# Kernel tuning notes

Measured on AMD Instinct MI355X. Metric: run time of the kernel, lower is better.

The kernel has to match this reference:

```python
import jax, jax.numpy as jnp
import numpy as np


def setup_inputs() -> dict:
    key = jax.random.key(0)
    k_x, k_m, k_w1, k_b1, k_w2, k_b2 = jax.random.split(key, 6)
    b, seq_len, d_in, d_out = 8, 4096, 1024, 512
    x = jax.random.normal(k_x, (b, seq_len, d_in), dtype=jnp.float32)
    # binary-ish mask in {0,1} as floats (torch code multiplies by mask)
    mask = (jax.random.uniform(k_m, (b, seq_len)) < 0.5).astype(jnp.float32)
    s1 = 1.0 / np.sqrt(d_in)
    s2 = 1.0 / np.sqrt(d_out)
    W_enc = jax.random.uniform(k_w1, (d_out, d_in), minval=-s1, maxval=s1, dtype=jnp.float32)
    b_enc = jax.random.uniform(k_b1, (d_out,), minval=-s1, maxval=s1, dtype=jnp.float32)
    W_dec = jax.random.uniform(k_w2, (d_in, d_out), minval=-s2, maxval=s2, dtype=jnp.float32)
    b_dec = jax.random.uniform(k_b2, (d_in,), minval=-s2, maxval=s2, dtype=jnp.float32)
    return {"x": x, "mask": mask, "W_enc": W_enc, "b_enc": b_enc, "W_dec": W_dec, "b_dec": b_dec}


def reference(x, mask, W_enc, b_enc, W_dec, b_dec):
    # per-step: v_t = v_{t-1} + relu(x_t @ W_enc^T + b_enc) * mask_t  -> additive scan == cumsum
    h = jax.nn.relu(jnp.einsum('bsd,od->bso', x, W_enc) + b_enc) * mask[:, :, None]  # [b,s,d_out]
    v_cum = jnp.cumsum(h, axis=1)  # [b,s,d_out]
    out_enc = jnp.einsum('bso,do->bsd', v_cum, W_dec) + b_dec  # decode every prefix state
    v = v_cum[:, -1, :]  # final accumulated state
    return (v, out_enc)
```

## Files before the change

### kernel.cpp

```cpp
#include <hip/hip_runtime.h>
#include <hip/hip_bf16.h>
#include <stdint.h>

typedef __bf16 bf16_t;
typedef __bf16 bf16x4 __attribute__((ext_vector_type(4)));
typedef __bf16 bf16x8 __attribute__((ext_vector_type(8)));
typedef float  f32x4  __attribute__((ext_vector_type(4)));

__device__ __forceinline__ void gload_lds16(const void* g, void* l) {
  __builtin_amdgcn_global_load_lds(
      (__attribute__((address_space(1))) void*)g,
      (__attribute__((address_space(3))) void*)l, 16, 0, 0);
}

__global__ void cast_kernel(const float* __restrict__ in, bf16_t* __restrict__ out, int n4) {
  const int stride = gridDim.x * blockDim.x;
  for (int i = blockIdx.x * blockDim.x + threadIdx.x; i < n4; i += stride) {
    f32x4 v = reinterpret_cast<const f32x4*>(in)[i];
    bf16x4 o;
    o[0] = (bf16_t)v[0]; o[1] = (bf16_t)v[1]; o[2] = (bf16_t)v[2]; o[3] = (bf16_t)v[3];
    reinterpret_cast<bf16x4*>(out)[i] = o;
  }
}

__global__ void cast_weights(const float* __restrict__ a, bf16_t* __restrict__ oa,
                             const float* __restrict__ b, bf16_t* __restrict__ ob,
                             int n4each) {
  const int i = blockIdx.x * blockDim.x + threadIdx.x;
  const float* src; bf16_t* dst; int k;
  if (i < n4each) { src = a; dst = oa; k = i; }
  else            { src = b; dst = ob; k = i - n4each; }
  f32x4 v = reinterpret_cast<const f32x4*>(src)[k];
  bf16x4 o;
  o[0] = (bf16_t)v[0]; o[1] = (bf16_t)v[1]; o[2] = (bf16_t)v[2]; o[3] = (bf16_t)v[3];
  reinterpret_cast<bf16x4*>(dst)[k] = o;
}


#define PHASE_SYNC() do { \
  __builtin_amdgcn_s_barrier(); \
  asm volatile("s_waitcnt lgkmcnt(0)" ::: "memory"); \
  __builtin_amdgcn_sched_barrier(0); \
  __builtin_amdgcn_s_setprio(1); \
} while (0)

#define PHASE_END() do { \
  __builtin_amdgcn_s_setprio(0); \
  __builtin_amdgcn_s_barrier(); \
} while (0)

#define QUAD(RH, CH, BF) do { \
  _Pragma("unroll") \
  for (int fr = 0; fr < 4; ++fr) { \
    _Pragma("unroll") \
    for (int fc = 0; fc < 2; ++fc) { \
      acc[RH][CH][fr][fc] = __builtin_amdgcn_mfma_f32_16x16x32_bf16(a[fr][0], BF[fc][0], acc[RH][CH][fr][fc], 0, 0, 0); \
      acc[RH][CH][fr][fc] = __builtin_amdgcn_mfma_f32_16x16x32_bf16(a[fr][1], BF[fc][1], acc[RH][CH][fr][fc], 0, 0, 0); \
    } \
  } \
} while (0)

template<int EPI>
__global__ __launch_bounds__(512, 2) void gemm8p(
    const bf16_t* __restrict__ A, const bf16_t* __restrict__ B,
    const int K, const int N,
    const float* __restrict__ bias, const float* __restrict__ mask,
    const float* __restrict__ Padd,
    bf16_t* __restrict__ h_out, float* __restrict__ partials,
    float* __restrict__ outf)
{
  __shared__ __align__(16) char smem[131072];

  const int tid  = threadIdx.x;
  const int lane = tid & 63;
  const int w    = tid >> 6;
  const int wm   = w >> 2;
  const int wn   = w & 3;
  const long bm  = (long)blockIdx.x * 256;
  const long bn  = (long)blockIdx.y * 256;
  const int NT   = K >> 6;

  const int scol = (((lane & 7) ^ (lane >> 3)) << 3);
  const int fcb0 = ((((lane >> 4)    ) ^ (lane & 7)) << 3);
  const int fcb1 = ((((lane >> 4) + 4) ^ (lane & 7)) << 3);

  f32x4  acc[2][2][4][2] = {};
  bf16x8 a[4][2], b0[2][2], b1[2][2];

  auto Albs = [&](int buf) { return (bf16_t*)(smem + buf * 65536); };
  auto Blbs = [&](int buf) { return (bf16_t*)(smem + buf * 65536 + 32768); };

  auto stageA = [&](int t, int h) {
    bf16_t* lb = Albs(t & 1);
    #pragma unroll
    for (int c = 0; c < 2; ++c) {
      const int r0 = h * 128 + (w * 2 + c) * 8;
      gload_lds16(A + (bm + r0 + (lane >> 3)) * (long)K + t * 64 + scol, lb + r0 * 64);
    }
  };
  auto stageB = [&](int t, int h) {
    bf16_t* lb = Blbs(t & 1);
    #pragma unroll
    for (int c = 0; c < 2; ++c) {
      const int r0 = h * 128 + (w * 2 + c) * 8;
      gload_lds16(B + (bn + r0 + (lane >> 3)) * (long)K + t * 64 + scol, lb + r0 * 64);
    }
  };
  auto loadA = [&](int buf, int rh) {
    const bf16_t* lb = Albs(buf);
    #pragma unroll
    for (int fr = 0; fr < 4; ++fr) {
      const int row = rh * 128 + wm * 64 + fr * 16 + (lane & 15);
      a[fr][0] = *reinterpret_cast<const bf16x8*>(lb + row * 64 + fcb0);
      a[fr][1] = *reinterpret_cast<const bf16x8*>(lb + row * 64 + fcb1);
    }
  };
  auto loadB = [&](int buf, int ch, bf16x8 (&bf)[2][2]) {
    const bf16_t* lb = Blbs(buf);
    #pragma unroll
    for (int fc = 0; fc < 2; ++fc) {
      const int row = ch * 128 + wn * 32 + fc * 16 + (lane & 15);
      bf[fc][0] = *reinterpret_cast<const bf16x8*>(lb + row * 64 + fcb0);
      bf[fc][1] = *reinterpret_cast<const bf16x8*>(lb + row * 64 + fcb1);
    }
  };

  __builtin_amdgcn_sched_barrier(0);
  stageA(0, 0); stageA(0, 1); stageB(0, 0); stageB(0, 1);
  stageA(1, 0); stageB(1, 0); stageA(1, 1);
  asm volatile("s_waitcnt vmcnt(6)" ::: "memory");
  __builtin_amdgcn_s_barrier();

  for (int t = 0; t < NT; ++t) {
    const int buf = t & 1;
    const bool s2 = (t + 2 < NT);
    const bool s1 = (t + 1 < NT);

    loadA(buf, 0);
    loadB(buf, 0, b0);
    if (s1) stageB(t + 1, 1);
    PHASE_SYNC(); QUAD(0, 0, b0); PHASE_END();

    loadB(buf, 1, b1);
    if (s2) stageA(t + 2, 0);
    PHASE_SYNC(); QUAD(0, 1, b1); PHASE_END();

    loadA(buf, 1);
    if (s2) stageB(t + 2, 0);
    PHASE_SYNC(); QUAD(1, 0, b0); PHASE_END();

    if (s2) stageA(t + 2, 1);
    PHASE_SYNC(); QUAD(1, 1, b1);
    __builtin_amdgcn_s_setprio(0);
    if (s2)      { asm volatile("s_waitcnt vmcnt(6)" ::: "memory"); }
    else if (s1) { asm volatile("s_waitcnt vmcnt(0)" ::: "memory"); }
    __builtin_amdgcn_s_barrier();
  }
  __builtin_amdgcn_sched_barrier(0);

  if (EPI == 0) {
    bf16_t* tile = (bf16_t*)smem;
    float bv[2][2];
    #pragma unroll
    for (int ch = 0; ch < 2; ++ch)
      #pragma unroll
      for (int fc = 0; fc < 2; ++fc)
        bv[ch][fc] = bias[bn + ch * 128 + wn * 32 + fc * 16 + (lane & 15)];

    #pragma unroll
    for (int rh = 0; rh < 2; ++rh)
      #pragma unroll
      for (int fr = 0; fr < 4; ++fr) {
        const int row0 = rh * 128 + wm * 64 + fr * 16 + ((lane >> 4) << 2);
        const f32x4 mv = *reinterpret_cast<const f32x4*>(&mask[bm + row0]);
        #pragma unroll
        for (int ch = 0; ch < 2; ++ch)
          #pragma unroll
          for (int fc = 0; fc < 2; ++fc) {
            const int col = ch * 128 + wn * 32 + fc * 16 + (lane & 15);
            #pragma unroll
            for (int e = 0; e < 4; ++e) {
              const int row = row0 + e;
              float hv = acc[rh][ch][fr][fc][e] + bv[ch][fc];
              hv = (hv > 0.f ? hv : 0.f) * mv[e];
              tile[row * 256 + (col ^ (((row >> 2) & 3) << 4))] = (bf16_t)hv;
            }
          }
      }
    __syncthreads();

    const int sub = tid >> 8;
    const int col = tid & 255;
    float run = 0.f;
    bf16_t* hp = h_out + (bm + sub * 128) * 512 + bn + col;
    #pragma unroll 4
    for (int s = 0; s < 128; ++s) {
      const int row = sub * 128 + s;
      run += (float)tile[row * 256 + (col ^ (((row >> 2) & 3) << 4))];
      hp[(long)s * 512] = (bf16_t)run;
    }
    partials[(blockIdx.x * 2 + sub) * 512 + bn + col] = run;
  } else {
    #pragma unroll
    for (int rh = 0; rh < 2; ++rh)
      #pragma unroll
      for (int ch = 0; ch < 2; ++ch)
        #pragma unroll
        for (int fc = 0; fc < 2; ++fc) {
          const long gc = bn + ch * 128 + wn * 32 + fc * 16 + (lane & 15);
          const float pv = Padd[(blockIdx.x * 2 + rh) * (long)N + gc];
          #pragma unroll
          for (int fr = 0; fr < 4; ++fr) {
            const long gr = bm + rh * 128 + wm * 64 + fr * 16 + ((lane >> 4) << 2);
            #pragma unroll
            for (int e = 0; e < 4; ++e)
              outf[(gr + e) * (long)N + gc] = acc[rh][ch][fr][fc][e] + pv;
          }
        }
  }
}

__global__ __launch_bounds__(256) void gemm_p(
    const bf16_t* __restrict__ A, const bf16_t* __restrict__ B,
    const int K, const int N,
    const float* __restrict__ bias,
    float* __restrict__ outf)
{
  __shared__ __align__(16) bf16_t As[2][128 * 64];
  __shared__ __align__(16) bf16_t Bs[2][128 * 64];

  const int tid  = threadIdx.x;
  const int lane = tid & 63;
  const int w    = tid >> 6;
  const int wm   = w >> 1, wn = w & 1;
  const long bm  = (long)blockIdx.x * 128;
  const long bn  = (long)blockIdx.y * 128;

  f32x4 acc[4][4] = {};

  const int srow = w * 32 + (lane >> 3);
  const int scol = (lane & 7) * 8;
  const bf16_t* Abase = A + (bm + srow) * (long)K + scol;
  const bf16_t* Bbase = B + (bn + srow) * (long)K + scol;

  auto stage = [&](bf16_t* da, bf16_t* db, int kt) {
    #pragma unroll
    for (int it = 0; it < 4; ++it) {
      gload_lds16(Abase + (long)it * 8 * K + kt, &da[(w * 32 + it * 8) * 64]);
      gload_lds16(Bbase + (long)it * 8 * K + kt, &db[(w * 32 + it * 8) * 64]);
    }
  };
  auto mfma_tile = [&](const bf16_t* Asb, const bf16_t* Bsb) {
    #pragma unroll
    for (int kk = 0; kk < 2; ++kk) {
      const int kof = kk * 32 + (lane >> 4) * 8;
      bf16x8 afr[4], bfr[4];
      #pragma unroll
      for (int i = 0; i < 4; ++i)
        afr[i] = *reinterpret_cast<const bf16x8*>(&Asb[(wm * 64 + i * 16 + (lane & 15)) * 64 + kof]);
      #pragma unroll
      for (int j = 0; j < 4; ++j)
        bfr[j] = *reinterpret_cast<const bf16x8*>(&Bsb[(wn * 64 + j * 16 + (lane & 15)) * 64 + kof]);
      #pragma unroll
      for (int i = 0; i < 4; ++i)
        #pragma unroll
        for (int j = 0; j < 4; ++j)
          acc[i][j] = __builtin_amdgcn_mfma_f32_16x16x32_bf16(afr[i], bfr[j], acc[i][j], 0, 0, 0);
    }
  };

  stage(As[0], Bs[0], 0);
  __syncthreads();
  int kt = 64;
  for (int p2 = 0; p2 < (K >> 7); ++p2) {
    if (kt < K) stage(As[1], Bs[1], kt);
    mfma_tile(As[0], Bs[0]);
    __syncthreads();
    kt += 64;
    if (kt < K) stage(As[0], Bs[0], kt);
    mfma_tile(As[1], Bs[1]);
    __syncthreads();
    kt += 64;
  }

  #pragma unroll
  for (int j = 0; j < 4; ++j) {
    const long gc = bn + wn * 64 + j * 16 + (lane & 15);
    const float addv = bias[gc];
    #pragma unroll
    for (int i = 0; i < 4; ++i) {
      const long gr0 = bm + wm * 64 + i * 16 + ((lane >> 4) << 2);
      #pragma unroll
      for (int r = 0; r < 4; ++r)
        outf[(gr0 + r) * (long)N + gc] = acc[i][j][r] + addv;
    }
  }
}

__global__ void scan_chunks(const float* __restrict__ partials, bf16_t* __restrict__ prefixb,
                            float* __restrict__ v_out) {
  const int idx = blockIdx.x * blockDim.x + threadIdx.x;
  const int b = idx >> 9;
  const int o = idx & 511;
  float run = 0.f;
  #pragma unroll
  for (int c = 0; c < 32; ++c) {
    const size_t off = ((size_t)(b * 32 + c)) * 512 + o;
    prefixb[off] = (bf16_t)run;
    run += partials[off];
  }
  v_out[idx] = run;
}

extern "C" void kernel_launch(void* const* d_in, const int* in_sizes, int n_in,
                              void* d_out, int out_size, void* d_ws, size_t ws_size,
                              hipStream_t stream) {
  const float* x     = (const float*)d_in[0];
  const float* mask  = (const float*)d_in[1];
  const float* W_enc = (const float*)d_in[2];
  const float* b_enc = (const float*)d_in[3];
  const float* W_dec = (const float*)d_in[4];
  const float* b_dec = (const float*)d_in[5];

  float* out     = (float*)d_out;
  float* v_out   = out;
  float* out_enc = out + 4096;

  char* ws = (char*)d_ws;
  bf16_t* xb       = (bf16_t*)ws;  ws += (size_t)32768 * 1024 * 2;
  bf16_t* Web      = (bf16_t*)ws;  ws += (size_t)512 * 1024 * 2;
  bf16_t* Wdb      = (bf16_t*)ws;  ws += (size_t)1024 * 512 * 2;
  bf16_t* h        = (bf16_t*)ws;  ws += (size_t)32768 * 512 * 2;
  float*  partials = (float*)ws;   ws += (size_t)256 * 512 * 4;
  bf16_t* prefixb  = (bf16_t*)ws;  ws += (size_t)256 * 512 * 2;
  float*  P        = (float*)ws;   ws += (size_t)256 * 1024 * 4;

  cast_kernel<<<2048, 256, 0, stream>>>(x, xb, 33554432 / 4);
  cast_weights<<<1024, 256, 0, stream>>>(W_enc, Web, W_dec, Wdb, 131072);

  gemm8p<0><<<dim3(128, 2), 512, 0, stream>>>(xb, Web, 1024, 512,
                                              b_enc, mask, nullptr, h, partials, nullptr);

  scan_chunks<<<16, 256, 0, stream>>>(partials, prefixb, v_out);

  gemm_p<<<dim3(2, 8), 256, 0, stream>>>(prefixb, Wdb, 512, 1024, b_dec, P);

  gemm8p<1><<<dim3(128, 4), 512, 0, stream>>>(h, Wdb, 512, 1024,
                                              nullptr, nullptr, P, nullptr, nullptr, out_enc);
}
```

Baseline: 163.7 us.

## Fuse fp32-to-bf16 cast of x into the encoder GEMM's LDS staging

Drops the separate cast kernel for x. The encoder GEMM now loads fp32 x tiles directly into LDS and converts them to bf16 while reading fragments. This removes a full write and re-read of a 64 MB bf16 copy of x. In exchange, the encoder kernel moves twice the bytes per A tile through LDS, single-buffers A with a restructured staging and waitcnt schedule, and does extra conversion work in the inner loop. The decoder GEMM also has its prefetch order and wait counts reshuffled.

```diff
diff --git a/kernel.cpp b/kernel.cpp
--- a/kernel.cpp
+++ b/kernel.cpp
@@ -11,16 +11,6 @@
   __builtin_amdgcn_global_load_lds(
       (__attribute__((address_space(1))) void*)g,
       (__attribute__((address_space(3))) void*)l, 16, 0, 0);
-}
-
-__global__ void cast_kernel(const float* __restrict__ in, bf16_t* __restrict__ out, int n4) {
-  const int stride = gridDim.x * blockDim.x;
-  for (int i = blockIdx.x * blockDim.x + threadIdx.x; i < n4; i += stride) {
-    f32x4 v = reinterpret_cast<const f32x4*>(in)[i];
-    bf16x4 o;
-    o[0] = (bf16_t)v[0]; o[1] = (bf16_t)v[1]; o[2] = (bf16_t)v[2]; o[3] = (bf16_t)v[3];
-    reinterpret_cast<bf16x4*>(out)[i] = o;
-  }
 }
 
 __global__ void cast_weights(const float* __restrict__ a, bf16_t* __restrict__ oa,
@@ -36,7 +26,6 @@
   reinterpret_cast<bf16x4*>(dst)[k] = o;
 }
 
-
 #define PHASE_SYNC() do { \
   __builtin_amdgcn_s_barrier(); \
   asm volatile("s_waitcnt lgkmcnt(0)" ::: "memory"); \
@@ -60,13 +49,161 @@
   } \
 } while (0)
 
-template<int EPI>
-__global__ __launch_bounds__(512, 2) void gemm8p(
+__global__ __launch_bounds__(512, 2) void gemm1_f8p(
+    const float* __restrict__ x, const bf16_t* __restrict__ Wenc,
+    const float* __restrict__ b_enc, const float* __restrict__ mask,
+    bf16_t* __restrict__ h_out, float* __restrict__ partials)
+{
+  __shared__ __align__(16) char smem[131072];
+  float* Af = (float*)smem;
+  auto Bl = [&](int buf) { return (bf16_t*)(smem + 65536 + buf * 32768); };
+
+  const int tid  = threadIdx.x;
+  const int lane = tid & 63;
+  const int w    = tid >> 6;
+  const int wm   = w >> 2;
+  const int wn   = w & 3;
+  const long bm  = (long)blockIdx.x * 256;
+  const long bn  = (long)blockIdx.y * 256;
+  const int NT   = 16;
+
+  f32x4  acc[2][2][4][2] = {};
+  bf16x8 a[4][2], b0[2][2], b1[2][2];
+
+  const int scolB = (((lane & 7) ^ (lane >> 3)) << 3);
+  auto stageB = [&](int t, int h) {
+    bf16_t* lb = Bl(t & 1);
+    #pragma unroll
+    for (int c = 0; c < 2; ++c) {
+      const int r0 = h * 128 + (w * 2 + c) * 8;
+      gload_lds16(Wenc + (bn + r0 + (lane >> 3)) * 1024 + t * 64 + scolB, lb + r0 * 64);
+    }
+  };
+  auto stageA = [&](int t, int h) {
+    #pragma unroll
+    for (int c = 0; c < 4; ++c) {
+      const int r0  = h * 128 + w * 16 + c * 4;
+      const int row = r0 + (lane >> 4);
+      const int sblk = (lane & 15) ^ (row & 15);
+      gload_lds16(x + (bm + row) * 1024 + t * 64 + sblk * 4, Af + r0 * 64);
+    }
+  };
+  auto loadAf = [&](int rh) {
+    #pragma unroll
+    for (int fr = 0; fr < 4; ++fr) {
+      const int row = rh * 128 + wm * 64 + fr * 16 + (lane & 15);
+      const float* rp = Af + row * 64;
+      #pragma unroll
+      for (int kx = 0; kx < 2; ++kx) {
+        const int g0 = kx * 8 + (lane >> 4) * 2;
+        f32x4 lo = *reinterpret_cast<const f32x4*>(rp + (((g0    ) ^ (lane & 15)) << 2));
+        f32x4 hi = *reinterpret_cast<const f32x4*>(rp + (((g0 + 1) ^ (lane & 15)) << 2));
+        bf16x8 o;
+        #pragma unroll
+        for (int e = 0; e < 4; ++e) { o[e] = (bf16_t)lo[e]; o[e + 4] = (bf16_t)hi[e]; }
+        a[fr][kx] = o;
+      }
+    }
+  };
+  const int fcb0 = ((((lane >> 4)    ) ^ (lane & 7)) << 3);
+  const int fcb1 = ((((lane >> 4) + 4) ^ (lane & 7)) << 3);
+  auto loadB = [&](int buf, int ch, bf16x8 (&bf)[2][2]) {
+    const bf16_t* lb = Bl(buf);
+    #pragma unroll
+    for (int fc = 0; fc < 2; ++fc) {
+      const int row = ch * 128 + wn * 32 + fc * 16 + (lane & 15);
+      bf[fc][0] = *reinterpret_cast<const bf16x8*>(lb + row * 64 + fcb0);
+      bf[fc][1] = *reinterpret_cast<const bf16x8*>(lb + row * 64 + fcb1);
+    }
+  };
+
+  __builtin_amdgcn_sched_barrier(0);
+  stageA(0, 0); stageA(0, 1); stageB(0, 0); stageB(0, 1);
+  stageB(1, 0); stageB(1, 1);
+  asm volatile("s_waitcnt vmcnt(4)" ::: "memory");
+  __builtin_amdgcn_s_barrier();
+
+  for (int t = 0; t < NT; ++t) {
+    const int buf = t & 1;
+    const bool g1 = (t + 1 < NT);
+    const bool g2 = (t + 2 < NT);
+
+    loadAf(0); loadB(buf, 0, b0);
+    PHASE_SYNC(); QUAD(0, 0, b0); PHASE_END();
+
+    loadB(buf, 1, b1);
+    if (g1) stageA(t + 1, 0);
+    if (g2) stageB(t + 2, 0);
+    PHASE_SYNC(); QUAD(0, 1, b1);
+    __builtin_amdgcn_s_setprio(0);
+    if (g2)      asm volatile("s_waitcnt vmcnt(6)" ::: "memory");
+    else if (g1) asm volatile("s_waitcnt vmcnt(4)" ::: "memory");
+    else         asm volatile("s_waitcnt vmcnt(0)" ::: "memory");
+    __builtin_amdgcn_s_barrier();
+
+    loadAf(1);
+    if (g2) stageB(t + 2, 1);
+    PHASE_SYNC(); QUAD(1, 0, b0); PHASE_END();
+
+    if (g1) stageA(t + 1, 1);
+    PHASE_SYNC(); QUAD(1, 1, b1);
+    __builtin_amdgcn_s_setprio(0);
+    if (g2)      asm volatile("s_waitcnt vmcnt(8)" ::: "memory");
+    else if (g1) asm volatile("s_waitcnt vmcnt(4)" ::: "memory");
+    else         asm volatile("s_waitcnt vmcnt(0)" ::: "memory");
+    __builtin_amdgcn_s_barrier();
+  }
+  asm volatile("s_waitcnt vmcnt(0) lgkmcnt(0)" ::: "memory");
+  __builtin_amdgcn_s_barrier();
+  __builtin_amdgcn_sched_barrier(0);
+
+  bf16_t* tile = (bf16_t*)smem;
+  float bv[2][2];
+  #pragma unroll
+  for (int ch = 0; ch < 2; ++ch)
+    #pragma unroll
+    for (int fc = 0; fc < 2; ++fc)
+      bv[ch][fc] = b_enc[bn + ch * 128 + wn * 32 + fc * 16 + (lane & 15)];
+
+  #pragma unroll
+  for (int rh = 0; rh < 2; ++rh)
+    #pragma unroll
+    for (int fr = 0; fr < 4; ++fr) {
+      const int row0 = rh * 128 + wm * 64 + fr * 16 + ((lane >> 4) << 2);
+      const f32x4 mv = *reinterpret_cast<const f32x4*>(&mask[bm + row0]);
+      #pragma unroll
+      for (int ch = 0; ch < 2; ++ch)
+        #pragma unroll
+        for (int fc = 0; fc < 2; ++fc) {
+          const int col = ch * 128 + wn * 32 + fc * 16 + (lane & 15);
+          #pragma unroll
+          for (int e = 0; e < 4; ++e) {
+            const int row = row0 + e;
+            float hv = acc[rh][ch][fr][fc][e] + bv[ch][fc];
+            hv = (hv > 0.f ? hv : 0.f) * mv[e];
+            tile[row * 256 + (col ^ (((row >> 2) & 3) << 4))] = (bf16_t)hv;
+          }
+        }
+    }
+  __syncthreads();
+
+  const int sub = tid >> 8;
+  const int col = tid & 255;
+  float run = 0.f;
+  bf16_t* hp = h_out + (bm + sub * 128) * 512 + bn + col;
+  #pragma unroll 4
+  for (int s = 0; s < 128; ++s) {
+    const int row = sub * 128 + s;
+    run += (float)tile[row * 256 + (col ^ (((row >> 2) & 3) << 4))];
+    hp[(long)s * 512] = (bf16_t)run;
+  }
+  partials[(blockIdx.x * 2 + sub) * 512 + bn + col] = run;
+}
+
+__global__ __launch_bounds__(512, 2) void gemm2_8p(
     const bf16_t* __restrict__ A, const bf16_t* __restrict__ B,
     const int K, const int N,
-    const float* __restrict__ bias, const float* __restrict__ mask,
     const float* __restrict__ Padd,
-    bf16_t* __restrict__ h_out, float* __restrict__ partials,
     float* __restrict__ outf)
 {
   __shared__ __align__(16) char smem[131072];
@@ -127,97 +264,50 @@
 
   __builtin_amdgcn_sched_barrier(0);
   stageA(0, 0); stageA(0, 1); stageB(0, 0); stageB(0, 1);
-  stageA(1, 0); stageB(1, 0); stageA(1, 1);
-  asm volatile("s_waitcnt vmcnt(6)" ::: "memory");
+  stageA(1, 0); stageA(1, 1); stageB(1, 0); stageB(1, 1);
+  asm volatile("s_waitcnt vmcnt(8)" ::: "memory");
   __builtin_amdgcn_s_barrier();
 
   for (int t = 0; t < NT; ++t) {
     const int buf = t & 1;
-    const bool s2 = (t + 2 < NT);
-    const bool s1 = (t + 1 < NT);
-
-    loadA(buf, 0);
-    loadB(buf, 0, b0);
-    if (s1) stageB(t + 1, 1);
+    const bool g2 = (t + 2 < NT);
+
+    loadA(buf, 0); loadB(buf, 0, b0);
     PHASE_SYNC(); QUAD(0, 0, b0); PHASE_END();
 
     loadB(buf, 1, b1);
-    if (s2) stageA(t + 2, 0);
+    if (g2) stageA(t + 2, 0);
     PHASE_SYNC(); QUAD(0, 1, b1); PHASE_END();
 
     loadA(buf, 1);
-    if (s2) stageB(t + 2, 0);
+    if (g2) stageB(t + 2, 0);
     PHASE_SYNC(); QUAD(1, 0, b0); PHASE_END();
 
-    if (s2) stageA(t + 2, 1);
+    if (g2) { stageA(t + 2, 1); stageB(t + 2, 1); }
     PHASE_SYNC(); QUAD(1, 1, b1);
     __builtin_amdgcn_s_setprio(0);
-    if (s2)      { asm volatile("s_waitcnt vmcnt(6)" ::: "memory"); }
-    else if (s1) { asm volatile("s_waitcnt vmcnt(0)" ::: "memory"); }
+    if (g2) asm volatile("s_waitcnt vmcnt(8)" ::: "memory");
+    else    asm volatile("s_waitcnt vmcnt(0)" ::: "memory");
     __builtin_amdgcn_s_barrier();
   }
   __builtin_amdgcn_sched_barrier(0);
 
-  if (EPI == 0) {
-    bf16_t* tile = (bf16_t*)smem;
-    float bv[2][2];
+  #pragma unroll
+  for (int rh = 0; rh < 2; ++rh)
     #pragma unroll
     for (int ch = 0; ch < 2; ++ch)
       #pragma unroll
-      for (int fc = 0; fc < 2; ++fc)
-        bv[ch][fc] = bias[bn + ch * 128 + wn * 32 + fc * 16 + (lane & 15)];
-
-    #pragma unroll
-    for (int rh = 0; rh < 2; ++rh)
-      #pragma unroll
-      for (int fr = 0; fr < 4; ++fr) {
-        const int row0 = rh * 128 + wm * 64 + fr * 16 + ((lane >> 4) << 2);
-        const f32x4 mv = *reinterpret_cast<const f32x4*>(&mask[bm + row0]);
+      for (int fc = 0; fc < 2; ++fc) {
+        const long gc = bn + ch * 128 + wn * 32 + fc * 16 + (lane & 15);
+        const float pv = Padd[(blockIdx.x * 2 + rh) * (long)N + gc];
         #pragma unroll
-        for (int ch = 0; ch < 2; ++ch)
+        for (int fr = 0; fr < 4; ++fr) {
+          const long gr = bm + rh * 128 + wm * 64 + fr * 16 + ((lane >> 4) << 2);
           #pragma unroll
-          for (int fc = 0; fc < 2; ++fc) {
-            const int col = ch * 128 + wn * 32 + fc * 16 + (lane & 15);
-            #pragma unroll
-            for (int e = 0; e < 4; ++e) {
-              const int row = row0 + e;
-              float hv = acc[rh][ch][fr][fc][e] + bv[ch][fc];
-              hv = (hv > 0.f ? hv : 0.f) * mv[e];
-              tile[row * 256 + (col ^ (((row >> 2) & 3) << 4))] = (bf16_t)hv;
-            }
-          }
+          for (int e = 0; e < 4; ++e)
+            outf[(gr + e) * (long)N + gc] = acc[rh][ch][fr][fc][e] + pv;
+        }
       }
-    __syncthreads();
-
-    const int sub = tid >> 8;
-    const int col = tid & 255;
-    float run = 0.f;
-    bf16_t* hp = h_out + (bm + sub * 128) * 512 + bn + col;
-    #pragma unroll 4
-    for (int s = 0; s < 128; ++s) {
-      const int row = sub * 128 + s;
-      run += (float)tile[row * 256 + (col ^ (((row >> 2) & 3) << 4))];
-      hp[(long)s * 512] = (bf16_t)run;
-    }
-    partials[(blockIdx.x * 2 + sub) * 512 + bn + col] = run;
-  } else {
-    #pragma unroll
-    for (int rh = 0; rh < 2; ++rh)
-      #pragma unroll
-      for (int ch = 0; ch < 2; ++ch)
-        #pragma unroll
-        for (int fc = 0; fc < 2; ++fc) {
-          const long gc = bn + ch * 128 + wn * 32 + fc * 16 + (lane & 15);
-          const float pv = Padd[(blockIdx.x * 2 + rh) * (long)N + gc];
-          #pragma unroll
-          for (int fr = 0; fr < 4; ++fr) {
-            const long gr = bm + rh * 128 + wm * 64 + fr * 16 + ((lane >> 4) << 2);
-            #pragma unroll
-            for (int e = 0; e < 4; ++e)
-              outf[(gr + e) * (long)N + gc] = acc[rh][ch][fr][fc][e] + pv;
-          }
-        }
-  }
 }
 
 __global__ __launch_bounds__(256) void gemm_p(
@@ -327,7 +417,6 @@
   float* out_enc = out + 4096;
 
   char* ws = (char*)d_ws;
-  bf16_t* xb       = (bf16_t*)ws;  ws += (size_t)32768 * 1024 * 2;
   bf16_t* Web      = (bf16_t*)ws;  ws += (size_t)512 * 1024 * 2;
   bf16_t* Wdb      = (bf16_t*)ws;  ws += (size_t)1024 * 512 * 2;
   bf16_t* h        = (bf16_t*)ws;  ws += (size_t)32768 * 512 * 2;
@@ -335,16 +424,13 @@
   bf16_t* prefixb  = (bf16_t*)ws;  ws += (size_t)256 * 512 * 2;
   float*  P        = (float*)ws;   ws += (size_t)256 * 1024 * 4;
 
-  cast_kernel<<<2048, 256, 0, stream>>>(x, xb, 33554432 / 4);
   cast_weights<<<1024, 256, 0, stream>>>(W_enc, Web, W_dec, Wdb, 131072);
 
-  gemm8p<0><<<dim3(128, 2), 512, 0, stream>>>(xb, Web, 1024, 512,
-                                              b_enc, mask, nullptr, h, partials, nullptr);
+  gemm1_f8p<<<dim3(128, 2), 512, 0, stream>>>(x, Web, b_enc, mask, h, partials);
 
   scan_chunks<<<16, 256, 0, stream>>>(partials, prefixb, v_out);
 
   gemm_p<<<dim3(2, 8), 256, 0, stream>>>(prefixb, Wdb, 512, 1024, b_dec, P);
 
-  gemm8p<1><<<dim3(128, 4), 512, 0, stream>>>(h, Wdb, 512, 1024,
-                                              nullptr, nullptr, P, nullptr, nullptr, out_enc);
-}
+  gemm2_8p<<<dim3(128, 4), 512, 0, stream>>>(h, Wdb, 512, 1024, P, out_enc);
+}
```

New measurement: 138.9 us. -15.2%, faster.

## Merge cast kernels and restage GEMM prefetch to two tiles ahead

Applied to the files above, without the earlier changes.

The x and weight casts are folded into one grid-stride kernel, which removes a launch. The GEMM prefetch schedule changes so that both halves of A and B for tile t+2 are staged within iteration t, replacing the mixed t+1/t+2 staging. The vmcnt thresholds are adjusted to match, and an lgkmcnt wait is added before the first quad. This aims to simplify and deepen the load pipeline, but more loads stay in flight, and wrong wait counts could stall the loop or break correctness.

```diff
diff --git a/kernel.cpp b/kernel.cpp
--- a/kernel.cpp
+++ b/kernel.cpp
@@ -13,29 +13,23 @@
       (__attribute__((address_space(3))) void*)l, 16, 0, 0);
 }
 
-__global__ void cast_kernel(const float* __restrict__ in, bf16_t* __restrict__ out, int n4) {
+__global__ void cast_all(const float* __restrict__ x, bf16_t* __restrict__ xb,
+                         const float* __restrict__ we, bf16_t* __restrict__ web,
+                         const float* __restrict__ wd, bf16_t* __restrict__ wdb) {
+  const int NX = 8388608;
+  const int NW = 131072;
   const int stride = gridDim.x * blockDim.x;
-  for (int i = blockIdx.x * blockDim.x + threadIdx.x; i < n4; i += stride) {
-    f32x4 v = reinterpret_cast<const f32x4*>(in)[i];
+  for (int i = blockIdx.x * blockDim.x + threadIdx.x; i < NX + 2 * NW; i += stride) {
+    const float* src; bf16_t* dst; int k;
+    if (i < NX)           { src = x;  dst = xb;  k = i; }
+    else if (i < NX + NW) { src = we; dst = web; k = i - NX; }
+    else                  { src = wd; dst = wdb; k = i - NX - NW; }
+    f32x4 v = reinterpret_cast<const f32x4*>(src)[k];
     bf16x4 o;
     o[0] = (bf16_t)v[0]; o[1] = (bf16_t)v[1]; o[2] = (bf16_t)v[2]; o[3] = (bf16_t)v[3];
-    reinterpret_cast<bf16x4*>(out)[i] = o;
-  }
-}
-
-__global__ void cast_weights(const float* __restrict__ a, bf16_t* __restrict__ oa,
-                             const float* __restrict__ b, bf16_t* __restrict__ ob,
-                             int n4each) {
-  const int i = blockIdx.x * blockDim.x + threadIdx.x;
-  const float* src; bf16_t* dst; int k;
-  if (i < n4each) { src = a; dst = oa; k = i; }
-  else            { src = b; dst = ob; k = i - n4each; }
-  f32x4 v = reinterpret_cast<const f32x4*>(src)[k];
-  bf16x4 o;
-  o[0] = (bf16_t)v[0]; o[1] = (bf16_t)v[1]; o[2] = (bf16_t)v[2]; o[3] = (bf16_t)v[3];
-  reinterpret_cast<bf16x4*>(dst)[k] = o;
-}
-
+    reinterpret_cast<bf16x4*>(dst)[k] = o;
+  }
+}
 
 #define PHASE_SYNC() do { \
   __builtin_amdgcn_s_barrier(); \
@@ -127,33 +121,31 @@
 
   __builtin_amdgcn_sched_barrier(0);
   stageA(0, 0); stageA(0, 1); stageB(0, 0); stageB(0, 1);
-  stageA(1, 0); stageB(1, 0); stageA(1, 1);
-  asm volatile("s_waitcnt vmcnt(6)" ::: "memory");
+  stageA(1, 0); stageA(1, 1); stageB(1, 0); stageB(1, 1);
+  asm volatile("s_waitcnt vmcnt(8)" ::: "memory");
   __builtin_amdgcn_s_barrier();
 
   for (int t = 0; t < NT; ++t) {
     const int buf = t & 1;
-    const bool s2 = (t + 2 < NT);
-    const bool s1 = (t + 1 < NT);
-
-    loadA(buf, 0);
-    loadB(buf, 0, b0);
-    if (s1) stageB(t + 1, 1);
+    const bool g2 = (t + 2 < NT);
+
+    loadA(buf, 0); loadB(buf, 0, b0);
+    asm volatile("s_waitcnt lgkmcnt(8)" ::: "memory");
     PHASE_SYNC(); QUAD(0, 0, b0); PHASE_END();
 
     loadB(buf, 1, b1);
-    if (s2) stageA(t + 2, 0);
+    if (g2) stageA(t + 2, 0);
     PHASE_SYNC(); QUAD(0, 1, b1); PHASE_END();
 
     loadA(buf, 1);
-    if (s2) stageB(t + 2, 0);
+    if (g2) stageB(t + 2, 0);
     PHASE_SYNC(); QUAD(1, 0, b0); PHASE_END();
 
-    if (s2) stageA(t + 2, 1);
+    if (g2) { stageA(t + 2, 1); stageB(t + 2, 1); }
     PHASE_SYNC(); QUAD(1, 1, b1);
     __builtin_amdgcn_s_setprio(0);
-    if (s2)      { asm volatile("s_waitcnt vmcnt(6)" ::: "memory"); }
-    else if (s1) { asm volatile("s_waitcnt vmcnt(0)" ::: "memory"); }
+    if (g2) asm volatile("s_waitcnt vmcnt(8)" ::: "memory");
+    else    asm volatile("s_waitcnt vmcnt(0)" ::: "memory");
     __builtin_amdgcn_s_barrier();
   }
   __builtin_amdgcn_sched_barrier(0);
@@ -335,8 +327,7 @@
   bf16_t* prefixb  = (bf16_t*)ws;  ws += (size_t)256 * 512 * 2;
   float*  P        = (float*)ws;   ws += (size_t)256 * 1024 * 4;
 
-  cast_kernel<<<2048, 256, 0, stream>>>(x, xb, 33554432 / 4);
-  cast_weights<<<1024, 256, 0, stream>>>(W_enc, Web, W_dec, Wdb, 131072);
+  cast_all<<<2048, 256, 0, stream>>>(x, xb, W_enc, Web, W_dec, Wdb);
 
   gemm8p<0><<<dim3(128, 2), 512, 0, stream>>>(xb, Web, 1024, 512,
                                               b_enc, mask, nullptr, h, partials, nullptr);
```

Result: no change. 162.0 us (-1.1%).
